# Kernel tuning notes

Hardware: AMD Instinct MI355X
Metric: run time of the kernel (lower is better)

The kernel has to match this reference:

```python
import jax, jax.numpy as jnp
import numpy as np

N_NODES = 1000
HIDDEN = 256
IN_DIM = 128
N_EDGES = 64000


def setup_inputs() -> dict:
    key = jax.random.key(0)
    ks = jax.random.split(key, 24)
    inp = {
        "x": jax.random.normal(ks[0], (N_NODES, IN_DIM), dtype=jnp.float32),
        "edge_index": jax.random.randint(ks[1], (2, N_EDGES), 0, N_NODES, dtype=jnp.int64),
    }
    dims = [(HIDDEN, 2 * IN_DIM)] + [(HIDDEN, 2 * HIDDEN)] * 4
    for l, (dout, din) in enumerate(dims):
        s0 = 1.0 / np.sqrt(din)
        s1 = 1.0 / np.sqrt(HIDDEN)
        inp[f"w{l}_0"] = jax.random.normal(ks[2 + 4 * l], (dout, din), dtype=jnp.float32) * s0
        inp[f"b{l}_0"] = jax.random.normal(ks[3 + 4 * l], (dout,), dtype=jnp.float32) * s0
        inp[f"w{l}_1"] = jax.random.normal(ks[4 + 4 * l], (HIDDEN, HIDDEN), dtype=jnp.float32) * s1
        inp[f"b{l}_1"] = jax.random.normal(ks[5 + 4 * l], (HIDDEN,), dtype=jnp.float32) * s1
    return inp


def _edge_conv(x, src, dst, w1, b1, w2, b2):
    # gather endpoint features per edge: [E, D]
    x_i = x[dst]  # destination (edge_index[1])
    x_j = x[src]  # source (edge_index[0])
    m = jnp.concatenate([x_i, x_j - x_i], axis=-1)  # [E, 2D]
    h = jax.nn.relu(m @ w1.T + b1) @ w2.T + b2      # 2-layer MLP, [E, HIDDEN]
    # scatter-max to destination nodes (include_self=False -> empty rows = 0)
    agg = jax.ops.segment_max(h, dst, num_segments=N_NODES)
    agg = jnp.where(jnp.isneginf(agg), jnp.zeros((), agg.dtype), agg)
    return jax.nn.relu(agg)


def reference(x, edge_index, w0_0, b0_0, w0_1, b0_1, w1_0, b1_0, w1_1, b1_1,
              w2_0, b2_0, w2_1, b2_1, w3_0, b3_0, w3_1, b3_1, w4_0, b4_0, w4_1, b4_1):
    src = edge_index[0]
    dst = edge_index[1]
    params = [(w0_0, b0_0, w0_1, b0_1), (w1_0, b1_0, w1_1, b1_1),
              (w2_0, b2_0, w2_1, b2_1), (w3_0, b3_0, w3_1, b3_1),
              (w4_0, b4_0, w4_1, b4_1)]
    h = x
    for (w1, b1, w2, b2) in params:
        h = _edge_conv(h, src, dst, w1, b1, w2, b2)
    return h
```

## Files before the change

### kernel.cpp

```cpp
#include <hip/hip_runtime.h>

#define NN 1000
#define NE 64000
#define HH 256

typedef _Float16 half8 __attribute__((ext_vector_type(8)));
typedef float floatx4 __attribute__((ext_vector_type(4)));

struct PrepArgs { const float* w0[5]; const float* w1[5]; };


template <int NK>
__device__ __forceinline__ void node_tile(const float* __restrict__ X,
                                          const _Float16* __restrict__ Wn,
                                          const float* __restrict__ b0,
                                          _Float16* __restrict__ out, int bid) {
    const int Kd = NK * 32;
    int t = threadIdx.x;
    int wave = t >> 6, lane = t & 63;
    int q = lane >> 4, mn = lane & 15;
    int m0 = (bid % 63) * 16;
    int n0 = (bid / 63) * 128 + wave * 32;
    int slice = (bid / 63) * 4 + wave;
    int rr = m0 + mn;
    if (rr >= NN) rr = NN - 1;

    half8 afa[NK];
    half8 bfa[NK][2];
#pragma unroll
    for (int kk = 0; kk < NK; kk++) {
        int ka = kk * 32 + q * 8;
        const float* p = X + (size_t)rr * Kd + ka;
        floatx4 x0 = *(const floatx4*)p;
        floatx4 x1 = *(const floatx4*)(p + 4);
        half8 aa;
#pragma unroll
        for (int j = 0; j < 4; j++) { aa[j] = (_Float16)x0[j]; aa[4 + j] = (_Float16)x1[j]; }
        afa[kk] = aa;
        bfa[kk][0] = *(const half8*)(Wn + (((slice * NK + kk) * 2 + 0) * 64 + lane) * 8);
        bfa[kk][1] = *(const half8*)(Wn + (((slice * NK + kk) * 2 + 1) * 64 + lane) * 8);
    }
    floatx4 acc[2] = {};
#pragma unroll
    for (int kk = 0; kk < NK; kk++) {
        acc[0] = __builtin_amdgcn_mfma_f32_16x16x32_f16(afa[kk], bfa[kk][0], acc[0], 0, 0, 0);
        acc[1] = __builtin_amdgcn_mfma_f32_16x16x32_f16(afa[kk], bfa[kk][1], acc[1], 0, 0, 0);
    }
#pragma unroll
    for (int nt = 0; nt < 2; nt++) {
        int col = n0 + nt * 16 + mn;
        float bias = (col < 256) ? b0[col] : 0.f;
#pragma unroll
        for (int r2 = 0; r2 < 4; r2++) {
            int orow = m0 + q * 4 + r2;
            if (orow < NN)
                out[(size_t)orow * 512 + col] = (_Float16)(acc[nt][r2] + bias);
        }
    }
}

__device__ __forceinline__ void node_tile0(const float* __restrict__ X,
                                           const float* __restrict__ w0,
                                           const float* __restrict__ b0,
                                           _Float16* __restrict__ out, int bid) {
    const int NK = 4;
    const int Kd = 128;
    int t = threadIdx.x;
    int wave = t >> 6, lane = t & 63;
    int q = lane >> 4, mn = lane & 15;
    int m0 = (bid % 63) * 16;
    int n0 = (bid / 63) * 128 + wave * 32;
    int slice = (bid / 63) * 4 + wave;
    int rr = m0 + mn;
    if (rr >= NN) rr = NN - 1;

    half8 afa[NK];
    half8 bfa[NK][2];
#pragma unroll
    for (int kk = 0; kk < NK; kk++) {
        int ka = kk * 32 + q * 8;
        const float* p = X + (size_t)rr * Kd + ka;
        floatx4 x0 = *(const floatx4*)p;
        floatx4 x1 = *(const floatx4*)(p + 4);
        half8 aa;
#pragma unroll
        for (int j = 0; j < 4; j++) { aa[j] = (_Float16)x0[j]; aa[4 + j] = (_Float16)x1[j]; }
        afa[kk] = aa;
#pragma unroll
        for (int nt = 0; nt < 2; nt++) {
            int n = slice * 32 + nt * 16 + mn;
            int k = kk * 32 + q * 8;
            half8 bb;
            if (n < 256) {
                const float* pa = w0 + (size_t)n * 256 + k;
                floatx4 a0 = *(const floatx4*)pa;
                floatx4 a1 = *(const floatx4*)(pa + 4);
                floatx4 c0 = *(const floatx4*)(pa + 128);
                floatx4 c1 = *(const floatx4*)(pa + 132);
#pragma unroll
                for (int j = 0; j < 4; j++) {
                    bb[j] = (_Float16)(a0[j] - c0[j]);
                    bb[4 + j] = (_Float16)(a1[j] - c1[j]);
                }
            } else {
                const float* pb = w0 + (size_t)(n - 256) * 256 + 128 + k;
                floatx4 c0 = *(const floatx4*)pb;
                floatx4 c1 = *(const floatx4*)(pb + 4);
#pragma unroll
                for (int j = 0; j < 4; j++) {
                    bb[j] = (_Float16)c0[j];
                    bb[4 + j] = (_Float16)c1[j];
                }
            }
            bfa[kk][nt] = bb;
        }
    }
    floatx4 acc[2] = {};
#pragma unroll
    for (int kk = 0; kk < NK; kk++) {
        acc[0] = __builtin_amdgcn_mfma_f32_16x16x32_f16(afa[kk], bfa[kk][0], acc[0], 0, 0, 0);
        acc[1] = __builtin_amdgcn_mfma_f32_16x16x32_f16(afa[kk], bfa[kk][1], acc[1], 0, 0, 0);
    }
#pragma unroll
    for (int nt = 0; nt < 2; nt++) {
        int col = n0 + nt * 16 + mn;
        float bias = (col < 256) ? b0[col] : 0.f;
#pragma unroll
        for (int r2 = 0; r2 < 4; r2++) {
            int orow = m0 + q * 4 + r2;
            if (orow < NN)
                out[(size_t)orow * 512 + col] = (_Float16)(acc[nt][r2] + bias);
        }
    }
}

__global__ __launch_bounds__(256) void k_pre1(PrepArgs pa,
                                              const int* __restrict__ ei,
                                              const float* __restrict__ X,
                                              const float* __restrict__ b0_0,
                                              _Float16* __restrict__ node_ab,
                                              _Float16* wnode, _Float16* w2h,
                                              int* cnts16, int* cursor,
                                              float* agg0, float* dout) {
    int bid = blockIdx.x;
    int t = threadIdx.x;
    if (bid < 16) {
        int* my = cnts16 + bid * 1024;
        for (int i = t; i < 1024; i += 256) my[i] = 0;
        __syncthreads();
        for (int e = bid * 256 + t; e < NE; e += 16 * 256)
            atomicAdd(&my[ei[NE + e] & 1023], 1);
    } else if (bid < 16 + 252) {
        node_tile0(X, pa.w0[0], b0_0, node_ab, bid - 16);
    } else {
        int gtid = (bid - 268) * 256 + t;
        int gs = 256 * 256;
        for (int i = gtid; i < 1024; i += gs) cursor[i] = 0;
        for (int l = 1; l < 5; l++) {
            const float* w0 = pa.w0[l];
            _Float16* wn = wnode + l * 131072;
            for (int i = gtid; i < 131072; i += gs) {
                int j = i & 7;
                int lane = (i >> 3) & 63;
                int nt = (i >> 9) & 1;
                int kk = (i >> 10) & 7;
                int slice = i >> 13;
                int mn = lane & 15, q = lane >> 4;
                int n = slice * 32 + nt * 16 + mn;
                int k = kk * 32 + q * 8 + j;
                float v = (n < 256) ? (w0[n * 512 + k] - w0[n * 512 + 256 + k])
                                    : w0[(n - 256) * 512 + 256 + k];
                wn[i] = (_Float16)v;
            }
        }
        for (int l = 0; l < 5; l++) {
            const float* w1 = pa.w1[l];
            _Float16* w2 = w2h + l * 65536;
            for (int i = gtid; i < 65536; i += gs) {
                int j = i & 7;
                int lane = (i >> 3) & 63;
                int nt = (i >> 9) & 3;
                int kk = (i >> 11) & 7;
                int ws = (i >> 14) & 3;
                int mn = lane & 15, q = lane >> 4;
                int row = ws * 64 + nt * 16 + mn;
                int col = kk * 32 + q * 8 + j;
                w2[i] = (_Float16)w1[row * 256 + col];
            }
        }
        floatx4 z = {0.f, 0.f, 0.f, 0.f};
        floatx4* p4 = (floatx4*)agg0;
        for (int i = gtid; i < 4 * NN * HH / 4; i += gs) p4[i] = z;
        floatx4* o4 = (floatx4*)dout;
        for (int i = gtid; i < NN * HH / 4; i += gs) o4[i] = z;
    }
}

__global__ __launch_bounds__(256) void k_scatter2(const int* __restrict__ ei,
                                                  const int* __restrict__ cnts16,
                                                  int* __restrict__ cursor,
                                                  int* __restrict__ ssrc,
                                                  int4* __restrict__ table) {
    __shared__ int sbase[1024];
    __shared__ int ssum[256];
    __shared__ int schk[256];
    int t = threadIdx.x;
    int base = t * 4;
    int c4[4]; int sum = 0;
#pragma unroll
    for (int j = 0; j < 4; j++) {
        int c = 0;
#pragma unroll
        for (int b = 0; b < 16; b++) c += cnts16[b * 1024 + base + j];
        c4[j] = c; sum += c;
    }
    ssum[t] = sum;
    int ch4[4]; int csum = 0;
#pragma unroll
    for (int j = 0; j < 4; j++) { ch4[j] = (c4[j] + 63) >> 6; csum += ch4[j]; }
    schk[t] = csum;
    __syncthreads();
    for (int d = 1; d < 256; d <<= 1) {
        int v1 = (t >= d) ? ssum[t - d] : 0;
        int v2 = (t >= d) ? schk[t - d] : 0;
        __syncthreads();
        ssum[t] += v1;
        schk[t] += v2;
        __syncthreads();
    }
    int run = (t > 0) ? ssum[t - 1] : 0;
#pragma unroll
    for (int j = 0; j < 4; j++) { sbase[base + j] = run; run += c4[j]; }
    __syncthreads();
    if (blockIdx.x == 0) {
        int crun = (t > 0) ? schk[t - 1] : 0;
#pragma unroll
        for (int j = 0; j < 4; j++) {
            int d = base + j, c = c4[j], st = sbase[base + j], nc = ch4[j];
            for (int k = 0; k < nc; k++) {
                int len = c - k * 64; if (len > 64) len = 64;
                table[crun + k] = make_int4(d, st + k * 64, len, nc == 1 ? 1 : 0);
            }
            crun += nc;
        }
        int nch = schk[255];
        for (int i = nch + t; i < 2048; i += 256) table[i] = make_int4(0, 0, 0, 0);
    }
    for (int e = blockIdx.x * 256 + t; e < NE; e += gridDim.x * 256) {
        int s = ei[e] & 1023, d = ei[NE + e] & 1023;
        int pos = sbase[d] + atomicAdd(&cursor[d], 1);
        if (pos < NE) ssrc[pos] = s;
    }
}

__global__ __launch_bounds__(256) void k_node(const float* __restrict__ agg_in,
                                              const _Float16* __restrict__ Wn,
                                              const float* __restrict__ b0,
                                              _Float16* __restrict__ out) {
    node_tile<8>(agg_in, Wn, b0, out, blockIdx.x);
}

__global__ __launch_bounds__(256, 4) void edge_gemm3(const _Float16* __restrict__ node_ab,
                          const int* __restrict__ ssrc,
                          const int4* __restrict__ table,
                          const _Float16* __restrict__ W2,
                          const float* __restrict__ b2,
                          float* __restrict__ agg) {
    __shared__ _Float16 h1[64 * 256];
    __shared__ int ssd[64];
    int4 ck = table[blockIdx.x];
    int len = ck.z;
    if (len == 0) return;
    int dst = ck.x, start = ck.y, sole = ck.w;
    int t = threadIdx.x;
    int wave = t >> 6, lane = t & 63;
    int q = lane >> 4, mn = lane & 15;
    const _Float16* W2w = W2 + wave * 16384;

    if (t < 64) ssd[t] = (t < len) ? ssrc[start + t] : 0;
    __syncthreads();
    {
        int s = lane & 31;
        int rh = lane >> 5;
        half8 av = *(const half8*)(node_ab + (size_t)dst * 512 + s * 8);
#pragma unroll
        for (int it = 0; it < 8; it++) {
            int row = it * 8 + wave * 2 + rh;
            half8 hv = {};
            if (row < len) {
                int sn = ssd[row];
                half8 bv = *(const half8*)(node_ab + (size_t)sn * 512 + 256 + s * 8);
                hv = av + bv;
#pragma unroll
                for (int j = 0; j < 8; j++) hv[j] = hv[j] > (_Float16)0 ? hv[j] : (_Float16)0;
            }
            int p = (s & ~7) | ((s ^ row) & 7);
            *(half8*)(&h1[row * 256 + p * 8]) = hv;
        }
    }
    __syncthreads();

    floatx4 acc[4][4] = {};
#pragma unroll
    for (int kk = 0; kk < 8; kk++) {
        half8 bf[4];
#pragma unroll
        for (int nt = 0; nt < 4; nt++)
            bf[nt] = *(const half8*)(W2w + (kk * 4 + nt) * 512 + lane * 8);
        half8 af[4];
#pragma unroll
        for (int mt = 0; mt < 4; mt++) {
            int r = mt * 16 + mn;
            int c = kk * 4 + q;
            int p = (c & ~7) | ((c ^ r) & 7);
            af[mt] = *(const half8*)(&h1[r * 256 + p * 8]);
        }
#pragma unroll
        for (int mt = 0; mt < 4; mt++)
#pragma unroll
            for (int nt = 0; nt < 4; nt++)
                acc[mt][nt] = __builtin_amdgcn_mfma_f32_16x16x32_f16(af[mt], bf[nt], acc[mt][nt], 0, 0, 0);
    }

    float m[4] = {-3.0e38f, -3.0e38f, -3.0e38f, -3.0e38f};
#pragma unroll
    for (int mt = 0; mt < 4; mt++) {
#pragma unroll
        for (int r2 = 0; r2 < 4; r2++) {
            int row = mt * 16 + q * 4 + r2;
            if (row < len) {
#pragma unroll
                for (int nt = 0; nt < 4; nt++) m[nt] = fmaxf(m[nt], acc[mt][nt][r2]);
            }
        }
    }
#pragma unroll
    for (int nt = 0; nt < 4; nt++) {
        m[nt] = fmaxf(m[nt], __shfl_xor(m[nt], 16, 64));
        m[nt] = fmaxf(m[nt], __shfl_xor(m[nt], 32, 64));
    }
    float v = (q == 0) ? m[0] : (q == 1) ? m[1] : (q == 2) ? m[2] : m[3];
    int col = wave * 64 + q * 16 + mn;
    v = v + b2[col];
    v = v > 0.f ? v : 0.f;
    float* p = agg + (size_t)dst * HH + col;
    if (sole) {
        *p = v;
    } else if (v > 0.f) {
        atomicMax((unsigned int*)p, __float_as_uint(v));
    }
}

extern "C" void kernel_launch(void* const* d_in, const int* in_sizes, int n_in,
                              void* d_out, int out_size, void* d_ws, size_t ws_size,
                              hipStream_t stream) {
    const float* x = (const float*)d_in[0];
    const int* ei = (const int*)d_in[1];
    PrepArgs pa;
    const float* b0s[5];
    const float* b1s[5];
    for (int l = 0; l < 5; l++) {
        pa.w0[l] = (const float*)d_in[2 + 4 * l];
        b0s[l] = (const float*)d_in[3 + 4 * l];
        pa.w1[l] = (const float*)d_in[4 + 4 * l];
        b1s[l] = (const float*)d_in[5 + 4 * l];
    }

    int* ssrc = (int*)d_ws;
    int* cnts16 = ssrc + NE;
    int* cursor = cnts16 + 16 * 1024;
    int4* table = (int4*)(cursor + 1024);
    _Float16* node_ab = (_Float16*)(table + 2048);
    float* agg0 = (float*)(node_ab + 1024 * 512);
    float* agg1 = agg0 + NN * HH;
    float* agg2 = agg1 + NN * HH;
    float* agg3 = agg2 + NN * HH;
    _Float16* wnode = (_Float16*)(agg3 + NN * HH);
    _Float16* w2h = wnode + 5 * 131072;

    hipLaunchKernelGGL(k_pre1, dim3(524), dim3(256), 0, stream,
                       pa, ei, x, b0s[0], node_ab, wnode, w2h,
                       cnts16, cursor, agg0, (float*)d_out);
    hipLaunchKernelGGL(k_scatter2, dim3(NE / 256), dim3(256), 0, stream,
                       ei, cnts16, cursor, ssrc, table);

    float* aggs[5] = {agg0, agg1, agg2, agg3, (float*)d_out};
    for (int l = 0; l < 5; l++) {
        hipLaunchKernelGGL(edge_gemm3, dim3(2048), dim3(256), 0, stream,
                           node_ab, ssrc, table, w2h + (size_t)l * 65536, b1s[l], aggs[l]);
        if (l < 4)
            hipLaunchKernelGGL(k_node, dim3(252), dim3(256), 0, stream,
                               aggs[l], wnode + (size_t)(l + 1) * 131072, b0s[l + 1], node_ab);
    }
}
```

Before: 234.3 us.

## Make edge GEMM persistent with register-resident W2 across 16 waves

The edge MLP second-layer kernel goes from 2048 blocks of 4 waves to 256 blocks of 16 waves. Each block now loops over 8 destination chunks, and each wave keeps its 16-column slice of W2 in registers for the whole kernel. Before, every block reloaded W2 from global or L2 memory for every chunk, and this change is meant to remove that traffic. In exchange it uses only 256 blocks with one tile per wave and adds a __syncthreads per chunk, so per-chunk MFMA density drops and gather latency may be less hidden.

```diff
diff --git a/kernel.cpp b/kernel.cpp
--- a/kernel.cpp
+++ b/kernel.cpp
@@ -260,94 +260,86 @@
     node_tile<8>(agg_in, Wn, b0, out, blockIdx.x);
 }
 
-__global__ __launch_bounds__(256, 4) void edge_gemm3(const _Float16* __restrict__ node_ab,
+__global__ __launch_bounds__(1024, 4) void edge_gemm4(const _Float16* __restrict__ node_ab,
                           const int* __restrict__ ssrc,
                           const int4* __restrict__ table,
                           const _Float16* __restrict__ W2,
                           const float* __restrict__ b2,
                           float* __restrict__ agg) {
     __shared__ _Float16 h1[64 * 256];
-    __shared__ int ssd[64];
-    int4 ck = table[blockIdx.x];
-    int len = ck.z;
-    if (len == 0) return;
-    int dst = ck.x, start = ck.y, sole = ck.w;
     int t = threadIdx.x;
     int wave = t >> 6, lane = t & 63;
     int q = lane >> 4, mn = lane & 15;
-    const _Float16* W2w = W2 + wave * 16384;
-
-    if (t < 64) ssd[t] = (t < len) ? ssrc[start + t] : 0;
-    __syncthreads();
-    {
-        int s = lane & 31;
-        int rh = lane >> 5;
-        half8 av = *(const half8*)(node_ab + (size_t)dst * 512 + s * 8);
-#pragma unroll
-        for (int it = 0; it < 8; it++) {
-            int row = it * 8 + wave * 2 + rh;
-            half8 hv = {};
-            if (row < len) {
-                int sn = ssd[row];
-                half8 bv = *(const half8*)(node_ab + (size_t)sn * 512 + 256 + s * 8);
-                hv = av + bv;
-#pragma unroll
-                for (int j = 0; j < 8; j++) hv[j] = hv[j] > (_Float16)0 ? hv[j] : (_Float16)0;
-            }
-            int p = (s & ~7) | ((s ^ row) & 7);
-            *(half8*)(&h1[row * 256 + p * 8]) = hv;
-        }
-    }
-    __syncthreads();
-
-    floatx4 acc[4][4] = {};
-#pragma unroll
-    for (int kk = 0; kk < 8; kk++) {
-        half8 bf[4];
-#pragma unroll
-        for (int nt = 0; nt < 4; nt++)
-            bf[nt] = *(const half8*)(W2w + (kk * 4 + nt) * 512 + lane * 8);
-        half8 af[4];
+    int s = lane & 31;
+    int rp = t >> 5;
+
+    const _Float16* Wb = W2 + (wave >> 2) * 16384 + (wave & 3) * 512 + (size_t)lane * 8;
+    half8 w2r[8];
+#pragma unroll
+    for (int kk = 0; kk < 8; kk++)
+        w2r[kk] = *(const half8*)(Wb + kk * 2048);
+    float bias = b2[wave * 16 + mn];
+
+    for (int i = 0; i < 8; i++) {
+        int4 ck = table[blockIdx.x + i * 256];
+        int len = ck.z;
+        if (len == 0) continue;
+        int dst = ck.x, start = ck.y, sole = ck.w;
+
+        __syncthreads();
+        {
+            half8 av = *(const half8*)(node_ab + (size_t)dst * 512 + s * 8);
+#pragma unroll
+            for (int rr = 0; rr < 2; rr++) {
+                int row = rp * 2 + rr;
+                half8 hv = {};
+                if (row < len) {
+                    int sn = ssrc[start + row];
+                    half8 bv = *(const half8*)(node_ab + (size_t)sn * 512 + 256 + s * 8);
+                    hv = av + bv;
+#pragma unroll
+                    for (int j = 0; j < 8; j++) hv[j] = hv[j] > (_Float16)0 ? hv[j] : (_Float16)0;
+                }
+                int p = (s & ~7) | ((s ^ row) & 7);
+                *(half8*)(&h1[row * 256 + p * 8]) = hv;
+            }
+        }
+        __syncthreads();
+
+        floatx4 acc[4] = {};
+#pragma unroll
+        for (int kk = 0; kk < 8; kk++) {
+#pragma unroll
+            for (int mt = 0; mt < 4; mt++) {
+                int r = mt * 16 + mn;
+                int c = kk * 4 + q;
+                int p = (c & ~7) | ((c ^ r) & 7);
+                half8 af = *(const half8*)(&h1[r * 256 + p * 8]);
+                acc[mt] = __builtin_amdgcn_mfma_f32_16x16x32_f16(af, w2r[kk], acc[mt], 0, 0, 0);
+            }
+        }
+
+        float m = -3.0e38f;
 #pragma unroll
         for (int mt = 0; mt < 4; mt++) {
-            int r = mt * 16 + mn;
-            int c = kk * 4 + q;
-            int p = (c & ~7) | ((c ^ r) & 7);
-            af[mt] = *(const half8*)(&h1[r * 256 + p * 8]);
-        }
-#pragma unroll
-        for (int mt = 0; mt < 4; mt++)
-#pragma unroll
-            for (int nt = 0; nt < 4; nt++)
-                acc[mt][nt] = __builtin_amdgcn_mfma_f32_16x16x32_f16(af[mt], bf[nt], acc[mt][nt], 0, 0, 0);
-    }
-
-    float m[4] = {-3.0e38f, -3.0e38f, -3.0e38f, -3.0e38f};
-#pragma unroll
-    for (int mt = 0; mt < 4; mt++) {
-#pragma unroll
-        for (int r2 = 0; r2 < 4; r2++) {
-            int row = mt * 16 + q * 4 + r2;
-            if (row < len) {
-#pragma unroll
-                for (int nt = 0; nt < 4; nt++) m[nt] = fmaxf(m[nt], acc[mt][nt][r2]);
-            }
-        }
-    }
-#pragma unroll
-    for (int nt = 0; nt < 4; nt++) {
-        m[nt] = fmaxf(m[nt], __shfl_xor(m[nt], 16, 64));
-        m[nt] = fmaxf(m[nt], __shfl_xor(m[nt], 32, 64));
-    }
-    float v = (q == 0) ? m[0] : (q == 1) ? m[1] : (q == 2) ? m[2] : m[3];
-    int col = wave * 64 + q * 16 + mn;
-    v = v + b2[col];
-    v = v > 0.f ? v : 0.f;
-    float* p = agg + (size_t)dst * HH + col;
-    if (sole) {
-        *p = v;
-    } else if (v > 0.f) {
-        atomicMax((unsigned int*)p, __float_as_uint(v));
+#pragma unroll
+            for (int r2 = 0; r2 < 4; r2++) {
+                int row = mt * 16 + q * 4 + r2;
+                if (row < len) m = fmaxf(m, acc[mt][r2]);
+            }
+        }
+        m = fmaxf(m, __shfl_xor(m, 16, 64));
+        m = fmaxf(m, __shfl_xor(m, 32, 64));
+        if (q == 0) {
+            float v = m + bias;
+            v = v > 0.f ? v : 0.f;
+            float* p = agg + (size_t)dst * HH + wave * 16 + mn;
+            if (sole) {
+                *p = v;
+            } else if (v > 0.f) {
+                atomicMax((unsigned int*)p, __float_as_uint(v));
+            }
+        }
     }
 }
 
@@ -386,7 +378,7 @@
 
     float* aggs[5] = {agg0, agg1, agg2, agg3, (float*)d_out};
     for (int l = 0; l < 5; l++) {
-        hipLaunchKernelGGL(edge_gemm3, dim3(2048), dim3(256), 0, stream,
+        hipLaunchKernelGGL(edge_gemm4, dim3(256), dim3(1024), 0, stream,
                            node_ab, ssrc, table, w2h + (size_t)l * 65536, b1s[l], aggs[l]);
         if (l < 4)
             hipLaunchKernelGGL(k_node, dim3(252), dim3(256), 0, stream,
```

Measured after the change: 263.2 us. 1.12x slower.
